# Kernel tuning notes

Hardware: AMD Instinct MI355X
Metric: run time of the kernel (lower is better)

## Reference

```python
import jax, jax.numpy as jnp
import numpy as np

DK = 64  # head dim = n_features // n_heads = 512 // 8


def setup_inputs() -> dict:
    key = jax.random.key(0)
    ks = jax.random.split(key, 6)
    B, N, D = 2, 4096, 512
    feature = jax.random.normal(ks[0], (B, N, D), dtype=jnp.float32)
    Sh = jax.random.normal(ks[1], (B, N, N), dtype=jnp.float32)
    Sw = jax.random.normal(ks[2], (B, N, N), dtype=jnp.float32)
    # torch Linear weights are [out, in]; xavier-uniform init
    lim = np.sqrt(6.0 / (D + DK)).astype(np.float32)
    wq_w = jax.random.uniform(ks[3], (DK, D), jnp.float32, -lim, lim)
    wk_w = jax.random.uniform(ks[4], (DK, D), jnp.float32, -lim, lim)
    wv_w = jax.random.uniform(ks[5], (DK, D), jnp.float32, -lim, lim)
    zb = jnp.zeros((DK,), jnp.float32)
    return {"feature": feature, "Sh": Sh, "Sw": Sw,
            "wq_w": wq_w, "wq_b": zb, "wk_w": wk_w, "wk_b": zb,
            "wv_w": wv_w, "wv_b": zb}


def reference(feature, Sh, Sw, wq_w, wq_b, wk_w, wk_b, wv_w, wv_b):
    # Linear projections (torch: x @ W.T + b)
    Q = jnp.einsum('bnd,kd->bnk', feature, wq_w) + wq_b  # [B,N,dk]
    K = jnp.einsum('bnd,kd->bnk', feature, wk_w) + wk_b  # [B,N,dk]
    V = jnp.einsum('bnd,kd->bnk', feature, wv_w) + wv_b  # [B,N,dv]
    sqrt_dk = jnp.sqrt(jnp.float32(Q.shape[-1]))
    # scores = (QK^T + Sh + Sw) / sqrt(dk)  -- biases added BEFORE scaling,
    # exactly as in attnFunc
    A = (jnp.einsum('bqk,bnk->bqn', Q, K) + Sh + Sw) / sqrt_dk  # [B,N,N]
    A = jax.nn.softmax(A, axis=-1)
    return jnp.einsum('bqn,bnk->bqk', A, V)  # [B,N,dv]
```

## Files before the change

kernel.cpp:

```cpp
#include <hip/hip_runtime.h>
#include <hip/hip_bf16.h>


typedef short bf16x8 __attribute__((ext_vector_type(8)));
typedef short bf16x4 __attribute__((ext_vector_type(4)));
typedef float f32x4  __attribute__((ext_vector_type(4)));

#if __has_builtin(__builtin_amdgcn_exp2f)
#define EXP2F(x) __builtin_amdgcn_exp2f(x)
#else
#define EXP2F(x) exp2f(x)
#endif
#if __has_builtin(__builtin_amdgcn_rcpf)
#define RCPF(x) __builtin_amdgcn_rcpf(x)
#else
#define RCPF(x) (1.0f / (x))
#endif

__device__ __forceinline__ f32x4 mfma16(bf16x8 a, bf16x8 b, f32x4 c) {
  return __builtin_amdgcn_mfma_f32_16x16x32_bf16(a, b, c, 0, 0, 0);
}
__device__ __forceinline__ short f2b(float x) {
  __hip_bfloat16 h = __float2bfloat16(x);
  return __builtin_bit_cast(short, h);
}
__device__ __forceinline__ float b2f(short s) {
  return __bfloat162float(__builtin_bit_cast(__hip_bfloat16, s));
}
__device__ __forceinline__ void split_hl(float x, short& h, short& l) {
  __hip_bfloat16 bh = __float2bfloat16(x);
  h = __builtin_bit_cast(short, bh);
  l = f2b(x - __bfloat162float(bh));
}

__global__ void wcvt_kernel(const float* __restrict__ wq, const float* __restrict__ wk,
                            const float* __restrict__ wv,
                            short* __restrict__ wh, short* __restrict__ wl) {
  int idx = (blockIdx.x * 256 + threadIdx.x) * 4;
  int p = idx >> 15;
  int off = idx & 32767;
  const float* src = (p == 0) ? wq : (p == 1) ? wk : wv;
  f32x4 v = *(const f32x4*)(src + off);
  bf16x4 h, l;
#pragma unroll
  for (int j = 0; j < 4; ++j) { short hh, ll; split_hl(v[j], hh, ll); h[j] = hh; l[j] = ll; }
  *(bf16x4*)(wh + p * 32768 + off) = h;
  *(bf16x4*)(wl + p * 32768 + off) = l;
}

__global__ __launch_bounds__(256) void proj_kernel(
    const float* __restrict__ feat, const short* __restrict__ wh, const short* __restrict__ wl,
    const float* __restrict__ bq, const float* __restrict__ bk, const float* __restrict__ bv,
    short* __restrict__ Qh, short* __restrict__ Ql,
    short* __restrict__ Kh, short* __restrict__ Kl, short* __restrict__ Vt) {
  const int lane = threadIdx.x & 63, wave = threadIdx.x >> 6;
  const int lq = lane & 15, quad = lane >> 4;
  const int wid = blockIdx.x * 4 + wave;
  const int p = wid >> 9, rg = wid & 511;
  const int rbase = rg * 16;
  const float Cs = 0.18033688011112042f;

  f32x4 acc[4];
#pragma unroll
  for (int t = 0; t < 4; ++t) acc[t] = (f32x4){0.f, 0.f, 0.f, 0.f};

  const float* frow = feat + (size_t)(rbase + lq) * 512 + quad * 8;
  const int wrow = p * 64;
  for (int ks = 0; ks < 16; ++ks) {
    f32x4 f0 = *(const f32x4*)(frow + ks * 32);
    f32x4 f1 = *(const f32x4*)(frow + ks * 32 + 4);
    bf16x8 fh, fl;
#pragma unroll
    for (int j = 0; j < 4; ++j) {
      short hh, ll;
      split_hl(f0[j], hh, ll); fh[j] = hh; fl[j] = ll;
      split_hl(f1[j], hh, ll); fh[j + 4] = hh; fl[j + 4] = ll;
    }
#pragma unroll
    for (int t = 0; t < 4; ++t) {
      const int wo = (wrow + t * 16 + lq) * 512 + ks * 32 + quad * 8;
      bf16x8 wfh = *(const bf16x8*)(wh + wo);
      bf16x8 wfl = *(const bf16x8*)(wl + wo);
      acc[t] = mfma16(fh, wfh, acc[t]);
      acc[t] = mfma16(fl, wfh, acc[t]);
      acc[t] = mfma16(fh, wfl, acc[t]);
    }
  }
  const int b = rbase >> 12, rloc = rbase & 4095;
  if (p == 0) {
#pragma unroll
    for (int t = 0; t < 4; ++t) {
      const int dk = t * 16 + lq;
      const float bb = bq[dk];
#pragma unroll
      for (int r = 0; r < 4; ++r) {
        const int row = rbase + 4 * quad + r;
        short h, l;
        split_hl((acc[t][r] + bb) * Cs, h, l);
        Qh[row * 64 + dk] = h; Ql[row * 64 + dk] = l;
      }
    }
  } else if (p == 1) {
#pragma unroll
    for (int t = 0; t < 4; ++t) {
      const int dk = t * 16 + lq;
      const float bb = bk[dk];
#pragma unroll
      for (int r = 0; r < 4; ++r) {
        const int row = rbase + 4 * quad + r;
        short h, l;
        split_hl(acc[t][r] + bb, h, l);
        Kh[row * 64 + dk] = h; Kl[row * 64 + dk] = l;
      }
    }
  } else {
#pragma unroll
    for (int t = 0; t < 4; ++t) {
      const int dk = t * 16 + lq;
      const float bb = bv[dk];
      bf16x4 vpack;
#pragma unroll
      for (int r = 0; r < 4; ++r) vpack[r] = f2b(acc[t][r] + bb);
      *(bf16x4*)(Vt + (size_t)(b * 64 + dk) * 4096 + rloc + 4 * quad) = vpack;
    }
  }
}

__global__ __launch_bounds__(256, 4) void attn_kernel(
    const float* __restrict__ Sh, const float* __restrict__ Sw,
    const short* __restrict__ Qh, const short* __restrict__ Ql,
    const short* __restrict__ Kh, const short* __restrict__ Vt,
    float* __restrict__ Opart, float* __restrict__ lpart) {
  __shared__ short Plds[4][16][40];
  __shared__ short BiasLds[4][2][16][36];
  const int bid = blockIdx.x;
  const int sp = bid & 7, qt = (bid >> 3) & 63, b = bid >> 9;
  const int tid = threadIdx.x;
  const int wave = tid >> 6, lane = tid & 63, lq = lane & 15, quad = lane >> 4;
  const int qbase = qt * 64 + wave * 16;
  const float Cs = 0.18033688011112042f;

  const float* shp = Sh + (size_t)(b * 4096 + qbase) * 4096 + sp * 512;
  const float* swp = Sw + (size_t)(b * 4096 + qbase) * 4096 + sp * 512;
  const int lrow = lane >> 3;
  const int lcol = (lane & 7) * 4;

  f32x4 sa[2], sc[2];
#pragma unroll
  for (int j = 0; j < 2; ++j) {
    const size_t off = (size_t)(j * 8 + lrow) * 4096 + lcol;
    sa[j] = __builtin_nontemporal_load((const f32x4*)(shp + off));
    sc[j] = __builtin_nontemporal_load((const f32x4*)(swp + off));
  }

  const int qidx = (b * 4096 + qbase + lq) * 64 + quad * 8;
  const bf16x8 qfh0 = *(const bf16x8*)(Qh + qidx);
  const bf16x8 qfh1 = *(const bf16x8*)(Qh + qidx + 32);
  const bf16x8 qfl0 = *(const bf16x8*)(Ql + qidx);
  const bf16x8 qfl1 = *(const bf16x8*)(Ql + qidx + 32);

  f32x4 accO[4];
#pragma unroll
  for (int u = 0; u < 4; ++u) accO[u] = (f32x4){0.f, 0.f, 0.f, 0.f};
  float lsum = 0.f;
  short* pw = &Plds[wave][0][0];
  short* bw = &BiasLds[wave][0][0][0];
  const short* vbase = Vt + (size_t)b * 64 * 4096;

#pragma unroll 2
  for (int it = 0; it < 16; ++it) {
    const int cur = it & 1;
    short* bwc = bw + cur * 576;

#pragma unroll
    for (int j = 0; j < 2; ++j) {
      f32x4 s = (sa[j] + sc[j]) * Cs;
      bf16x4 pk;
#pragma unroll
      for (int r = 0; r < 4; ++r) pk[r] = f2b(s[r]);
      *(bf16x4*)(bwc + (j * 8 + lrow) * 36 + lcol) = pk;
    }

    const int kb = sp * 512 + it * 32;
    bf16x8 kh0[2], kh1[2];
#pragma unroll
    for (int t = 0; t < 2; ++t) {
      const int kidx = (b * 4096 + kb + t * 16 + lq) * 64 + quad * 8;
      kh0[t] = *(const bf16x8*)(Kh + kidx);
      kh1[t] = *(const bf16x8*)(Kh + kidx + 32);
    }
    bf16x8 vf[4];
#pragma unroll
    for (int u = 0; u < 4; ++u)
      vf[u] = *(const bf16x8*)(vbase + (size_t)(u * 16 + lq) * 4096 + kb + quad * 8);
    __builtin_amdgcn_sched_barrier(0);

    if (it < 15) {
#pragma unroll
      for (int j = 0; j < 2; ++j) {
        const size_t off = (size_t)(j * 8 + lrow) * 4096 + (it + 1) * 32 + lcol;
        sa[j] = __builtin_nontemporal_load((const f32x4*)(shp + off));
        sc[j] = __builtin_nontemporal_load((const f32x4*)(swp + off));
      }
    }
    __builtin_amdgcn_sched_barrier(0);

    f32x4 accS[2];
#pragma unroll
    for (int t = 0; t < 2; ++t) accS[t] = (f32x4){0.f, 0.f, 0.f, 0.f};
#pragma unroll
    for (int t = 0; t < 2; ++t) {
      accS[t] = mfma16(kh0[t], qfh0, accS[t]);
      accS[t] = mfma16(kh1[t], qfh1, accS[t]);
      accS[t] = mfma16(kh0[t], qfl0, accS[t]);
      accS[t] = mfma16(kh1[t], qfl1, accS[t]);
    }

#pragma unroll
    for (int t = 0; t < 2; ++t) {
      const bf16x4 bb = *(const bf16x4*)(bwc + lq * 36 + 16 * t + 4 * quad);
      bf16x4 pk;
#pragma unroll
      for (int r = 0; r < 4; ++r) {
        float s = accS[t][r] + b2f(bb[r]);
        float p = EXP2F(s);
        lsum += p;
        pk[r] = f2b(p);
      }
      *(bf16x4*)(pw + lq * 40 + 16 * t + 4 * quad) = pk;
    }

    const bf16x8 pa = *(const bf16x8*)(pw + lq * 40 + quad * 8);
#pragma unroll
    for (int u = 0; u < 4; ++u) accO[u] = mfma16(pa, vf[u], accO[u]);
  }

  lsum += __shfl_xor(lsum, 16, 64);
  lsum += __shfl_xor(lsum, 32, 64);

  const int orowW = sp * 8192 + b * 4096 + qbase;
  if (quad == 0) lpart[orowW + lq] = lsum;
#pragma unroll
  for (int u = 0; u < 4; ++u)
#pragma unroll
    for (int r = 0; r < 4; ++r)
      Opart[(size_t)(orowW + 4 * quad + r) * 64 + u * 16 + lq] = accO[u][r];
}

__global__ void combine_kernel(const float* __restrict__ Opart, const float* __restrict__ lpart,
                               float* __restrict__ out) {
  const int g = blockIdx.x * 256 + threadIdx.x;
  const int row = g >> 4;
  f32x4 o = (f32x4){0.f, 0.f, 0.f, 0.f};
  float l = 0.f;
#pragma unroll
  for (int s = 0; s < 8; ++s) {
    o += __builtin_nontemporal_load((const f32x4*)(Opart + (size_t)s * 524288 + g * 4));
    l += lpart[s * 8192 + row];
  }
  const float rl = RCPF(l);
  *(f32x4*)(out + g * 4) = o * rl;
}

extern "C" void kernel_launch(void* const* d_in, const int* in_sizes, int n_in,
                              void* d_out, int out_size, void* d_ws, size_t ws_size,
                              hipStream_t stream) {
  const float* feature = (const float*)d_in[0];
  const float* Sh = (const float*)d_in[1];
  const float* Sw = (const float*)d_in[2];
  const float* wq = (const float*)d_in[3];
  const float* bq = (const float*)d_in[4];
  const float* wk = (const float*)d_in[5];
  const float* bk = (const float*)d_in[6];
  const float* wv = (const float*)d_in[7];
  const float* bv = (const float*)d_in[8];

  char* ws = (char*)d_ws;
  const size_t MB = 1u << 20;
  short* Qh = (short*)(ws + 0 * MB);
  short* Ql = (short*)(ws + 1 * MB);
  short* Kh = (short*)(ws + 2 * MB);
  short* Kl = (short*)(ws + 3 * MB);
  short* Vt = (short*)(ws + 4 * MB);
  short* wh = (short*)(ws + 5 * MB);
  short* wl = (short*)(ws + 5 * MB + 262144);
  float* lpart = (float*)(ws + 5 * MB + 524288);
  float* Opart = (float*)(ws + 6 * MB);

  wcvt_kernel<<<96, 256, 0, stream>>>(wq, wk, wv, wh, wl);
  proj_kernel<<<384, 256, 0, stream>>>(feature, wh, wl, bq, bk, bv, Qh, Ql, Kh, Kl, Vt);
  attn_kernel<<<1024, 256, 0, stream>>>(Sh, Sw, Qh, Ql, Kh, Vt, Opart, lpart);
  combine_kernel<<<512, 256, 0, stream>>>(Opart, lpart, (float*)d_out);
}
```

Measured before the change: 351.5 us.

## Warp-specialize attention: producer waves stream Sh+Sw bias into LDS ring

Block size doubles to 512 threads. Four extra producer waves load the fp32 Sh and Sw tiles with deep register prefetch, fold them into a scaled bf16 bias, and write it into a two-slot LDS ring. They signal each half with workgroup-scoped release flags, and the consumer waves spin on those flags before running the QK/softmax/PV MFMA loop. The aim is to separate the memory-bound bias streaming from MMA work so more loads stay in flight. The cost is extra LDS, larger blocks that may lower occupancy, and spin-wait overhead, and the consumers cannot start until a whole 256-column half is ready.

```diff
diff --git a/kernel.cpp b/kernel.cpp
--- a/kernel.cpp
+++ b/kernel.cpp
@@ -126,33 +126,56 @@
   }
 }
 
-__global__ __launch_bounds__(256, 4) void attn_kernel(
+__global__ __launch_bounds__(512, 4) void attn_kernel(
     const float* __restrict__ Sh, const float* __restrict__ Sw,
     const short* __restrict__ Qh, const short* __restrict__ Ql,
     const short* __restrict__ Kh, const short* __restrict__ Vt,
     float* __restrict__ Opart, float* __restrict__ lpart) {
+  __shared__ short Ring[4][2][16][264];
   __shared__ short Plds[4][16][40];
-  __shared__ short BiasLds[4][2][16][36];
+  __shared__ int ready[4][2];
   const int bid = blockIdx.x;
   const int sp = bid & 7, qt = (bid >> 3) & 63, b = bid >> 9;
   const int tid = threadIdx.x;
   const int wave = tid >> 6, lane = tid & 63, lq = lane & 15, quad = lane >> 4;
+  const float Cs = 0.18033688011112042f;
+
+  if (wave < 4 && lane < 2) ready[wave][lane] = 0;
+  __syncthreads();
+
+  if (wave >= 4) {
+    const int pw = wave - 4;
+    const int qbase = qt * 64 + pw * 16;
+    const float* shs = Sh + (size_t)(b * 4096 + qbase) * 4096 + sp * 512 + lane * 4;
+    const float* sws = Sw + (size_t)(b * 4096 + qbase) * 4096 + sp * 512 + lane * 4;
+    short* ring = &Ring[pw][0][0][0];
+#pragma unroll
+    for (int sl = 0; sl < 2; ++sl) {
+      const size_t so = (size_t)sl * 256;
+      f32x4 ra[6], rb[6];
+#pragma unroll
+      for (int r = 0; r < 6; ++r) {
+        ra[r] = __builtin_nontemporal_load((const f32x4*)(shs + (size_t)r * 4096 + so));
+        rb[r] = __builtin_nontemporal_load((const f32x4*)(sws + (size_t)r * 4096 + so));
+      }
+#pragma unroll
+      for (int r = 0; r < 16; ++r) {
+        f32x4 s = (ra[r % 6] + rb[r % 6]) * Cs;
+        bf16x4 pk;
+#pragma unroll
+        for (int j = 0; j < 4; ++j) pk[j] = f2b(s[j]);
+        *(bf16x4*)(ring + (sl * 16 + r) * 264 + lane * 4) = pk;
+        if (r + 6 < 16) {
+          ra[r % 6] = __builtin_nontemporal_load((const f32x4*)(shs + (size_t)(r + 6) * 4096 + so));
+          rb[r % 6] = __builtin_nontemporal_load((const f32x4*)(sws + (size_t)(r + 6) * 4096 + so));
+        }
+      }
+      __hip_atomic_store(&ready[pw][sl], 1, __ATOMIC_RELEASE, __HIP_MEMORY_SCOPE_WORKGROUP);
+    }
+    return;
+  }
+
   const int qbase = qt * 64 + wave * 16;
-  const float Cs = 0.18033688011112042f;
-
-  const float* shp = Sh + (size_t)(b * 4096 + qbase) * 4096 + sp * 512;
-  const float* swp = Sw + (size_t)(b * 4096 + qbase) * 4096 + sp * 512;
-  const int lrow = lane >> 3;
-  const int lcol = (lane & 7) * 4;
-
-  f32x4 sa[2], sc[2];
-#pragma unroll
-  for (int j = 0; j < 2; ++j) {
-    const size_t off = (size_t)(j * 8 + lrow) * 4096 + lcol;
-    sa[j] = __builtin_nontemporal_load((const f32x4*)(shp + off));
-    sc[j] = __builtin_nontemporal_load((const f32x4*)(swp + off));
-  }
-
   const int qidx = (b * 4096 + qbase + lq) * 64 + quad * 8;
   const bf16x8 qfh0 = *(const bf16x8*)(Qh + qidx);
   const bf16x8 qfh1 = *(const bf16x8*)(Qh + qidx + 32);
@@ -163,76 +186,57 @@
 #pragma unroll
   for (int u = 0; u < 4; ++u) accO[u] = (f32x4){0.f, 0.f, 0.f, 0.f};
   float lsum = 0.f;
-  short* pw = &Plds[wave][0][0];
-  short* bw = &BiasLds[wave][0][0][0];
+  short* pw_ = &Plds[wave][0][0];
   const short* vbase = Vt + (size_t)b * 64 * 4096;
 
-#pragma unroll 2
-  for (int it = 0; it < 16; ++it) {
-    const int cur = it & 1;
-    short* bwc = bw + cur * 576;
-
-#pragma unroll
-    for (int j = 0; j < 2; ++j) {
-      f32x4 s = (sa[j] + sc[j]) * Cs;
-      bf16x4 pk;
-#pragma unroll
-      for (int r = 0; r < 4; ++r) pk[r] = f2b(s[r]);
-      *(bf16x4*)(bwc + (j * 8 + lrow) * 36 + lcol) = pk;
-    }
-
-    const int kb = sp * 512 + it * 32;
-    bf16x8 kh0[2], kh1[2];
-#pragma unroll
-    for (int t = 0; t < 2; ++t) {
-      const int kidx = (b * 4096 + kb + t * 16 + lq) * 64 + quad * 8;
-      kh0[t] = *(const bf16x8*)(Kh + kidx);
-      kh1[t] = *(const bf16x8*)(Kh + kidx + 32);
-    }
-    bf16x8 vf[4];
-#pragma unroll
-    for (int u = 0; u < 4; ++u)
-      vf[u] = *(const bf16x8*)(vbase + (size_t)(u * 16 + lq) * 4096 + kb + quad * 8);
-    __builtin_amdgcn_sched_barrier(0);
-
-    if (it < 15) {
-#pragma unroll
-      for (int j = 0; j < 2; ++j) {
-        const size_t off = (size_t)(j * 8 + lrow) * 4096 + (it + 1) * 32 + lcol;
-        sa[j] = __builtin_nontemporal_load((const f32x4*)(shp + off));
-        sc[j] = __builtin_nontemporal_load((const f32x4*)(swp + off));
-      }
-    }
-    __builtin_amdgcn_sched_barrier(0);
-
-    f32x4 accS[2];
-#pragma unroll
-    for (int t = 0; t < 2; ++t) accS[t] = (f32x4){0.f, 0.f, 0.f, 0.f};
-#pragma unroll
-    for (int t = 0; t < 2; ++t) {
-      accS[t] = mfma16(kh0[t], qfh0, accS[t]);
-      accS[t] = mfma16(kh1[t], qfh1, accS[t]);
-      accS[t] = mfma16(kh0[t], qfl0, accS[t]);
-      accS[t] = mfma16(kh1[t], qfl1, accS[t]);
-    }
-
-#pragma unroll
-    for (int t = 0; t < 2; ++t) {
-      const bf16x4 bb = *(const bf16x4*)(bwc + lq * 36 + 16 * t + 4 * quad);
-      bf16x4 pk;
-#pragma unroll
-      for (int r = 0; r < 4; ++r) {
-        float s = accS[t][r] + b2f(bb[r]);
-        float p = EXP2F(s);
-        lsum += p;
-        pk[r] = f2b(p);
-      }
-      *(bf16x4*)(pw + lq * 40 + 16 * t + 4 * quad) = pk;
-    }
-
-    const bf16x8 pa = *(const bf16x8*)(pw + lq * 40 + quad * 8);
-#pragma unroll
-    for (int u = 0; u < 4; ++u) accO[u] = mfma16(pa, vf[u], accO[u]);
+  for (int sl = 0; sl < 2; ++sl) {
+    while (__hip_atomic_load(&ready[wave][sl], __ATOMIC_ACQUIRE, __HIP_MEMORY_SCOPE_WORKGROUP) == 0)
+      __builtin_amdgcn_s_sleep(2);
+    const short* biasb = &Ring[wave][sl][0][0];
+#pragma unroll
+    for (int cc = 0; cc < 8; ++cc) {
+      const int kb = sp * 512 + sl * 256 + cc * 32;
+      bf16x8 kh0[2], kh1[2];
+#pragma unroll
+      for (int t = 0; t < 2; ++t) {
+        const int kidx = (b * 4096 + kb + t * 16 + lq) * 64 + quad * 8;
+        kh0[t] = *(const bf16x8*)(Kh + kidx);
+        kh1[t] = *(const bf16x8*)(Kh + kidx + 32);
+      }
+      bf16x8 vf[4];
+#pragma unroll
+      for (int u = 0; u < 4; ++u)
+        vf[u] = *(const bf16x8*)(vbase + (size_t)(u * 16 + lq) * 4096 + kb + quad * 8);
+
+      f32x4 accS[2];
+#pragma unroll
+      for (int t = 0; t < 2; ++t) accS[t] = (f32x4){0.f, 0.f, 0.f, 0.f};
+#pragma unroll
+      for (int t = 0; t < 2; ++t) {
+        accS[t] = mfma16(kh0[t], qfh0, accS[t]);
+        accS[t] = mfma16(kh1[t], qfh1, accS[t]);
+        accS[t] = mfma16(kh0[t], qfl0, accS[t]);
+        accS[t] = mfma16(kh1[t], qfl1, accS[t]);
+      }
+
+#pragma unroll
+      for (int t = 0; t < 2; ++t) {
+        const bf16x4 bb = *(const bf16x4*)(biasb + lq * 264 + cc * 32 + 16 * t + 4 * quad);
+        bf16x4 pk;
+#pragma unroll
+        for (int r = 0; r < 4; ++r) {
+          float s = accS[t][r] + b2f(bb[r]);
+          float p = EXP2F(s);
+          lsum += p;
+          pk[r] = f2b(p);
+        }
+        *(bf16x4*)(pw_ + lq * 40 + 16 * t + 4 * quad) = pk;
+      }
+
+      const bf16x8 pa = *(const bf16x8*)(pw_ + lq * 40 + quad * 8);
+#pragma unroll
+      for (int u = 0; u < 4; ++u) accO[u] = mfma16(pa, vf[u], accO[u]);
+    }
   }
 
   lsum += __shfl_xor(lsum, 16, 64);
@@ -289,6 +293,6 @@
 
   wcvt_kernel<<<96, 256, 0, stream>>>(wq, wk, wv, wh, wl);
   proj_kernel<<<384, 256, 0, stream>>>(feature, wh, wl, bq, bk, bv, Qh, Ql, Kh, Kl, Vt);
-  attn_kernel<<<1024, 256, 0, stream>>>(Sh, Sw, Qh, Ql, Kh, Vt, Opart, lpart);
+  attn_kernel<<<1024, 512, 0, stream>>>(Sh, Sw, Qh, Ql, Kh, Vt, Opart, lpart);
   combine_kernel<<<512, 256, 0, stream>>>(Opart, lpart, (float*)d_out);
 }
```

New measurement: 362.9 us. +3.2%, slower.

## Add producer wave that streams Sh+Sw bias tiles into LDS with ready flags

Applied to the files above, without the earlier changes.

The attention kernel now launches 320 threads per block. A dedicated fifth wave loads the Sh and Sw fp32 bias tiles for the block's 64 rows, converts their scaled sum to bf16 and writes it into a full-width LDS buffer. It then signals each consumer wave through workgroup-scope atomic ready flags. The four compute waves no longer issue bias loads themselves and only read bias from LDS, which separates the memory stream from the MFMA work. The cost is a larger LDS footprint, lower occupancy (launch bounds drop to 2 blocks), and consumers spinning until their whole 16-row slab is ready, which reduces overlap.

```diff
diff --git a/kernel.cpp b/kernel.cpp
--- a/kernel.cpp
+++ b/kernel.cpp
@@ -126,34 +126,65 @@
   }
 }
 
-__global__ __launch_bounds__(256, 4) void attn_kernel(
+__global__ __launch_bounds__(320, 2) void attn_kernel(
     const float* __restrict__ Sh, const float* __restrict__ Sw,
     const short* __restrict__ Qh, const short* __restrict__ Ql,
     const short* __restrict__ Kh, const short* __restrict__ Vt,
     float* __restrict__ Opart, float* __restrict__ lpart) {
+  __shared__ short Bias[4][16][520];
   __shared__ short Plds[4][16][40];
-  __shared__ short BiasLds[4][2][16][36];
+  __shared__ int ready[4];
   const int bid = blockIdx.x;
-  const int sp = bid & 7, qt = (bid >> 3) & 63, b = bid >> 9;
+  const int sp = bid & 7, qtb = bid >> 3;
+  const int R = qtb * 64;
+  const int b = R >> 12;
   const int tid = threadIdx.x;
-  const int wave = tid >> 6, lane = tid & 63, lq = lane & 15, quad = lane >> 4;
-  const int qbase = qt * 64 + wave * 16;
+  const int wave = tid >> 6, lane = tid & 63;
   const float Cs = 0.18033688011112042f;
 
-  const float* shp = Sh + (size_t)(b * 4096 + qbase) * 4096 + sp * 512;
-  const float* swp = Sw + (size_t)(b * 4096 + qbase) * 4096 + sp * 512;
-  const int lrow = lane >> 3;
-  const int lcol = (lane & 7) * 4;
-
-  f32x4 sa[2], sc[2];
-#pragma unroll
-  for (int j = 0; j < 2; ++j) {
-    const size_t off = (size_t)(j * 8 + lrow) * 4096 + lcol;
-    sa[j] = __builtin_nontemporal_load((const f32x4*)(shp + off));
-    sc[j] = __builtin_nontemporal_load((const f32x4*)(swp + off));
-  }
-
-  const int qidx = (b * 4096 + qbase + lq) * 64 + quad * 8;
+  if (wave == 4 && lane < 4) ready[lane] = 0;
+  __syncthreads();
+
+  if (wave == 4) {
+    const float* shp = Sh + (size_t)R * 4096 + sp * 512;
+    const float* swp = Sw + (size_t)R * 4096 + sp * 512;
+    const int lo = lane * 4;
+
+#define LOADG(A, P, G)                                                                     \
+    A[0] = __builtin_nontemporal_load((const f32x4*)((P) + (size_t)(2 * (G)) * 4096 + lo));       \
+    A[1] = __builtin_nontemporal_load((const f32x4*)((P) + (size_t)(2 * (G)) * 4096 + 256 + lo)); \
+    A[2] = __builtin_nontemporal_load((const f32x4*)((P) + (size_t)(2 * (G) + 1) * 4096 + lo));   \
+    A[3] = __builtin_nontemporal_load((const f32x4*)((P) + (size_t)(2 * (G) + 1) * 4096 + 256 + lo));
+
+#define STOREG(A, C, G)                                                                    \
+    _Pragma("unroll")                                                                      \
+    for (int j = 0; j < 4; ++j) {                                                          \
+      f32x4 s = (A[j] + C[j]) * Cs;                                                        \
+      bf16x4 pk;                                                                           \
+      _Pragma("unroll")                                                                    \
+      for (int r = 0; r < 4; ++r) pk[r] = f2b(s[r]);                                       \
+      *(bf16x4*)(&Bias[(G) >> 3][(2 * (G) + (j >> 1)) & 15][(j & 1) * 256 + lo]) = pk;     \
+    }
+
+    f32x4 a0[4], c0[4], a1[4], c1[4];
+    LOADG(a0, shp, 0) LOADG(c0, swp, 0)
+    LOADG(a1, shp, 1) LOADG(c1, swp, 1)
+    for (int g = 0; g < 32; g += 2) {
+      STOREG(a0, c0, g)
+      if (g + 2 < 32) { LOADG(a0, shp, g + 2) LOADG(c0, swp, g + 2) }
+      STOREG(a1, c1, g + 1)
+      if (g + 3 < 32) { LOADG(a1, shp, g + 3) LOADG(c1, swp, g + 3) }
+      if (((g + 1) & 7) == 7)
+        __hip_atomic_store(&ready[(g + 1) >> 3], 1, __ATOMIC_RELEASE, __HIP_MEMORY_SCOPE_WORKGROUP);
+    }
+#undef LOADG
+#undef STOREG
+    return;
+  }
+
+  const int lq = lane & 15, quad = lane >> 4;
+  const int qbaseF = R + wave * 16;
+  const int qidx = (qbaseF + lq) * 64 + quad * 8;
   const bf16x8 qfh0 = *(const bf16x8*)(Qh + qidx);
   const bf16x8 qfh1 = *(const bf16x8*)(Qh + qidx + 32);
   const bf16x8 qfl0 = *(const bf16x8*)(Ql + qidx);
@@ -163,24 +194,15 @@
 #pragma unroll
   for (int u = 0; u < 4; ++u) accO[u] = (f32x4){0.f, 0.f, 0.f, 0.f};
   float lsum = 0.f;
-  short* pw = &Plds[wave][0][0];
-  short* bw = &BiasLds[wave][0][0][0];
+  short* pw_ = &Plds[wave][0][0];
+  const short* bw = &Bias[wave][0][0];
   const short* vbase = Vt + (size_t)b * 64 * 4096;
+
+  while (__hip_atomic_load(&ready[wave], __ATOMIC_ACQUIRE, __HIP_MEMORY_SCOPE_WORKGROUP) == 0)
+    __builtin_amdgcn_s_sleep(4);
 
 #pragma unroll 2
   for (int it = 0; it < 16; ++it) {
-    const int cur = it & 1;
-    short* bwc = bw + cur * 576;
-
-#pragma unroll
-    for (int j = 0; j < 2; ++j) {
-      f32x4 s = (sa[j] + sc[j]) * Cs;
-      bf16x4 pk;
-#pragma unroll
-      for (int r = 0; r < 4; ++r) pk[r] = f2b(s[r]);
-      *(bf16x4*)(bwc + (j * 8 + lrow) * 36 + lcol) = pk;
-    }
-
     const int kb = sp * 512 + it * 32;
     bf16x8 kh0[2], kh1[2];
 #pragma unroll
@@ -193,17 +215,6 @@
 #pragma unroll
     for (int u = 0; u < 4; ++u)
       vf[u] = *(const bf16x8*)(vbase + (size_t)(u * 16 + lq) * 4096 + kb + quad * 8);
-    __builtin_amdgcn_sched_barrier(0);
-
-    if (it < 15) {
-#pragma unroll
-      for (int j = 0; j < 2; ++j) {
-        const size_t off = (size_t)(j * 8 + lrow) * 4096 + (it + 1) * 32 + lcol;
-        sa[j] = __builtin_nontemporal_load((const f32x4*)(shp + off));
-        sc[j] = __builtin_nontemporal_load((const f32x4*)(swp + off));
-      }
-    }
-    __builtin_amdgcn_sched_barrier(0);
 
     f32x4 accS[2];
 #pragma unroll
@@ -218,7 +229,7 @@
 
 #pragma unroll
     for (int t = 0; t < 2; ++t) {
-      const bf16x4 bb = *(const bf16x4*)(bwc + lq * 36 + 16 * t + 4 * quad);
+      const bf16x4 bb = *(const bf16x4*)(bw + lq * 520 + it * 32 + 16 * t + 4 * quad);
       bf16x4 pk;
 #pragma unroll
       for (int r = 0; r < 4; ++r) {
@@ -227,10 +238,10 @@
         lsum += p;
         pk[r] = f2b(p);
       }
-      *(bf16x4*)(pw + lq * 40 + 16 * t + 4 * quad) = pk;
-    }
-
-    const bf16x8 pa = *(const bf16x8*)(pw + lq * 40 + quad * 8);
+      *(bf16x4*)(pw_ + lq * 40 + 16 * t + 4 * quad) = pk;
+    }
+
+    const bf16x8 pa = *(const bf16x8*)(pw_ + lq * 40 + quad * 8);
 #pragma unroll
     for (int u = 0; u < 4; ++u) accO[u] = mfma16(pa, vf[u], accO[u]);
   }
@@ -238,7 +249,7 @@
   lsum += __shfl_xor(lsum, 16, 64);
   lsum += __shfl_xor(lsum, 32, 64);
 
-  const int orowW = sp * 8192 + b * 4096 + qbase;
+  const int orowW = sp * 8192 + qbaseF;
   if (quad == 0) lpart[orowW + lq] = lsum;
 #pragma unroll
   for (int u = 0; u < 4; ++u)
@@ -289,6 +300,6 @@
 
   wcvt_kernel<<<96, 256, 0, stream>>>(wq, wk, wv, wh, wl);
   proj_kernel<<<384, 256, 0, stream>>>(feature, wh, wl, bq, bk, bv, Qh, Ql, Kh, Kl, Vt);
-  attn_kernel<<<1024, 256, 0, stream>>>(Sh, Sw, Qh, Ql, Kh, Vt, Opart, lpart);
+  attn_kernel<<<1024, 320, 0, stream>>>(Sh, Sw, Qh, Ql, Kh, Vt, Opart, lpart);
   combine_kernel<<<512, 256, 0, stream>>>(Opart, lpart, (float*)d_out);
 }
```

Measured after the change: 362.6 us. 3.2% more time.

## Precompute combined scaled bias in bf16 with separate prep kernel

Applied to the files above, without the earlier changes.

Adds a bias_prep_kernel that reads Sh and Sw once, sums and scales them, and writes a bf16 bias matrix to workspace. The attention kernel then loads this bf16 bias directly per lane, dropping the fp32 bias prefetch, the LDS staging buffer and the scheduling barriers. This simplifies and lightens the attention inner loop, but adds an extra full-size write and read of the bias through global memory plus another kernel launch.

```diff
diff --git a/kernel.cpp b/kernel.cpp
--- a/kernel.cpp
+++ b/kernel.cpp
@@ -126,32 +126,43 @@
   }
 }
 
+__global__ __launch_bounds__(256) void bias_prep_kernel(
+    const float* __restrict__ Sh, const float* __restrict__ Sw,
+    short* __restrict__ BiasBf) {
+  const float Cs = 0.18033688011112042f;
+  const int g = blockIdx.x * 256 + threadIdx.x;
+#pragma unroll
+  for (int it = 0; it < 16; it += 4) {
+    f32x4 a[4], c[4];
+#pragma unroll
+    for (int j = 0; j < 4; ++j) {
+      const size_t o = ((size_t)(it + j) * 524288 + g) * 4;
+      a[j] = __builtin_nontemporal_load((const f32x4*)(Sh + o));
+      c[j] = __builtin_nontemporal_load((const f32x4*)(Sw + o));
+    }
+#pragma unroll
+    for (int j = 0; j < 4; ++j) {
+      const size_t o = ((size_t)(it + j) * 524288 + g) * 4;
+      f32x4 s = (a[j] + c[j]) * Cs;
+      bf16x4 pk;
+#pragma unroll
+      for (int r = 0; r < 4; ++r) pk[r] = f2b(s[r]);
+      *(bf16x4*)(BiasBf + o) = pk;
+    }
+  }
+}
+
 __global__ __launch_bounds__(256, 4) void attn_kernel(
-    const float* __restrict__ Sh, const float* __restrict__ Sw,
+    const short* __restrict__ BiasBf,
     const short* __restrict__ Qh, const short* __restrict__ Ql,
     const short* __restrict__ Kh, const short* __restrict__ Vt,
     float* __restrict__ Opart, float* __restrict__ lpart) {
   __shared__ short Plds[4][16][40];
-  __shared__ short BiasLds[4][2][16][36];
   const int bid = blockIdx.x;
   const int sp = bid & 7, qt = (bid >> 3) & 63, b = bid >> 9;
   const int tid = threadIdx.x;
   const int wave = tid >> 6, lane = tid & 63, lq = lane & 15, quad = lane >> 4;
   const int qbase = qt * 64 + wave * 16;
-  const float Cs = 0.18033688011112042f;
-
-  const float* shp = Sh + (size_t)(b * 4096 + qbase) * 4096 + sp * 512;
-  const float* swp = Sw + (size_t)(b * 4096 + qbase) * 4096 + sp * 512;
-  const int lrow = lane >> 3;
-  const int lcol = (lane & 7) * 4;
-
-  f32x4 sa[2], sc[2];
-#pragma unroll
-  for (int j = 0; j < 2; ++j) {
-    const size_t off = (size_t)(j * 8 + lrow) * 4096 + lcol;
-    sa[j] = __builtin_nontemporal_load((const f32x4*)(shp + off));
-    sc[j] = __builtin_nontemporal_load((const f32x4*)(swp + off));
-  }
 
   const int qidx = (b * 4096 + qbase + lq) * 64 + quad * 8;
   const bf16x8 qfh0 = *(const bf16x8*)(Qh + qidx);
@@ -159,28 +170,17 @@
   const bf16x8 qfl0 = *(const bf16x8*)(Ql + qidx);
   const bf16x8 qfl1 = *(const bf16x8*)(Ql + qidx + 32);
 
+  const short* brow = BiasBf + (size_t)(b * 4096 + qbase + lq) * 4096 + sp * 512;
+
   f32x4 accO[4];
 #pragma unroll
   for (int u = 0; u < 4; ++u) accO[u] = (f32x4){0.f, 0.f, 0.f, 0.f};
   float lsum = 0.f;
-  short* pw = &Plds[wave][0][0];
-  short* bw = &BiasLds[wave][0][0][0];
+  short* pw_ = &Plds[wave][0][0];
   const short* vbase = Vt + (size_t)b * 64 * 4096;
 
 #pragma unroll 2
   for (int it = 0; it < 16; ++it) {
-    const int cur = it & 1;
-    short* bwc = bw + cur * 576;
-
-#pragma unroll
-    for (int j = 0; j < 2; ++j) {
-      f32x4 s = (sa[j] + sc[j]) * Cs;
-      bf16x4 pk;
-#pragma unroll
-      for (int r = 0; r < 4; ++r) pk[r] = f2b(s[r]);
-      *(bf16x4*)(bwc + (j * 8 + lrow) * 36 + lcol) = pk;
-    }
-
     const int kb = sp * 512 + it * 32;
     bf16x8 kh0[2], kh1[2];
 #pragma unroll
@@ -193,17 +193,8 @@
 #pragma unroll
     for (int u = 0; u < 4; ++u)
       vf[u] = *(const bf16x8*)(vbase + (size_t)(u * 16 + lq) * 4096 + kb + quad * 8);
-    __builtin_amdgcn_sched_barrier(0);
-
-    if (it < 15) {
-#pragma unroll
-      for (int j = 0; j < 2; ++j) {
-        const size_t off = (size_t)(j * 8 + lrow) * 4096 + (it + 1) * 32 + lcol;
-        sa[j] = __builtin_nontemporal_load((const f32x4*)(shp + off));
-        sc[j] = __builtin_nontemporal_load((const f32x4*)(swp + off));
-      }
-    }
-    __builtin_amdgcn_sched_barrier(0);
+    const bf16x4 bb0 = *(const bf16x4*)(brow + it * 32 + 4 * quad);
+    const bf16x4 bb1 = *(const bf16x4*)(brow + it * 32 + 16 + 4 * quad);
 
     f32x4 accS[2];
 #pragma unroll
@@ -218,7 +209,7 @@
 
 #pragma unroll
     for (int t = 0; t < 2; ++t) {
-      const bf16x4 bb = *(const bf16x4*)(bwc + lq * 36 + 16 * t + 4 * quad);
+      const bf16x4 bb = t ? bb1 : bb0;
       bf16x4 pk;
 #pragma unroll
       for (int r = 0; r < 4; ++r) {
@@ -227,10 +218,10 @@
         lsum += p;
         pk[r] = f2b(p);
       }
-      *(bf16x4*)(pw + lq * 40 + 16 * t + 4 * quad) = pk;
-    }
-
-    const bf16x8 pa = *(const bf16x8*)(pw + lq * 40 + quad * 8);
+      *(bf16x4*)(pw_ + lq * 40 + 16 * t + 4 * quad) = pk;
+    }
+
+    const bf16x8 pa = *(const bf16x8*)(pw_ + lq * 40 + quad * 8);
 #pragma unroll
     for (int u = 0; u < 4; ++u) accO[u] = mfma16(pa, vf[u], accO[u]);
   }
@@ -286,9 +277,11 @@
   short* wl = (short*)(ws + 5 * MB + 262144);
   float* lpart = (float*)(ws + 5 * MB + 524288);
   float* Opart = (float*)(ws + 6 * MB);
+  short* BiasBf = (short*)(ws + 24 * MB);
 
   wcvt_kernel<<<96, 256, 0, stream>>>(wq, wk, wv, wh, wl);
   proj_kernel<<<384, 256, 0, stream>>>(feature, wh, wl, bq, bk, bv, Qh, Ql, Kh, Kl, Vt);
-  attn_kernel<<<1024, 256, 0, stream>>>(Sh, Sw, Qh, Ql, Kh, Vt, Opart, lpart);
+  bias_prep_kernel<<<2048, 256, 0, stream>>>(Sh, Sw, BiasBf);
+  attn_kernel<<<1024, 256, 0, stream>>>(BiasBf, Qh, Ql, Kh, Vt, Opart, lpart);
   combine_kernel<<<512, 256, 0, stream>>>(Opart, lpart, (float*)d_out);
 }
```

Result: slower. 398.2 us (+13.3%).
